# Performance work log

Hardware: AMD Instinct MI355X
Metric: run time of the kernel (lower is better)

Reference implementation:

```python
import jax, jax.numpy as jnp
import numpy as np

N_HEAD = 16

def setup_inputs() -> dict:
    key = jax.random.key(0)
    k1, k2, k3, k4, k5 = jax.random.split(key, 5)
    B, S, D = 2, 2048, 1024
    return {
        "hidden_states": jax.random.normal(k1, (B, S, D), jnp.float32),
        "w_attn": jax.random.normal(k2, (D, 3 * D), jnp.float32) * 0.02,
        "b_attn": jax.random.normal(k3, (3 * D,), jnp.float32) * 0.02,
        "w_proj": jax.random.normal(k4, (D, D), jnp.float32) * 0.02,
        "b_proj": jax.random.normal(k5, (D,), jnp.float32) * 0.02,
    }

def reference(hidden_states, w_attn, b_attn, w_proj, b_proj):
    B, S, D = hidden_states.shape
    H = N_HEAD
    Dh = D // H
    qkv = hidden_states @ w_attn + b_attn              # [B,S,3D]
    q, k, v = jnp.split(qkv, 3, axis=-1)
    def split_heads(x):
        return x.reshape(B, S, H, Dh).transpose(0, 2, 1, 3)  # [B,H,S,Dh]
    q, k, v = split_heads(q), split_heads(k), split_heads(v)
    # scale=True: divide by sqrt(head_dim) (v.size(-1))
    scores = jnp.einsum("bhqd,bhkd->bhqk", q, k) / jnp.sqrt(jnp.float32(Dh))
    attn = jax.nn.softmax(scores, axis=-1)             # [B,H,S,S]
    out = jnp.einsum("bhqk,bhkd->bhqd", attn, v)       # [B,H,S,Dh]
    out = out.transpose(0, 2, 1, 3).reshape(B, S, D)   # merge heads
    return out @ w_proj + b_proj
```

## Files before the change

### kernel.cpp

```cpp
#include <hip/hip_runtime.h>
#include <hip/hip_bf16.h>

typedef __attribute__((ext_vector_type(8))) short bf16x8;
typedef __attribute__((ext_vector_type(4))) float f32x4;
typedef __attribute__((ext_vector_type(16))) float f32x16;

#define LOG2E 1.4426950408889634f

__device__ inline unsigned short f2bf(float f) {
  union { float f; unsigned u; } x; x.f = f;
  unsigned u = x.u;
  unsigned r = u + 0x7FFFu + ((u >> 16) & 1u);
  return (unsigned short)(r >> 16);
}

__device__ inline unsigned cvtpk(float lo, float hi) {
  unsigned r;
  asm("v_cvt_pk_bf16_f32 %0, %1, %2" : "=v"(r) : "v"(lo), "v"(hi));
  return r;
}

__device__ inline void gload16(const unsigned short* g, unsigned short* l) {
  __builtin_amdgcn_global_load_lds(
      (const __attribute__((address_space(1))) unsigned int*)g,
      (__attribute__((address_space(3))) unsigned int*)l, 16, 0, 0);
}

template <int J>
__device__ inline bf16x8 pack_pfrag(f32x16 p) {
  int X, Y, Z, W;
  asm("v_cvt_pk_bf16_f32 %0, %1, %2" : "=v"(X) : "v"(p[J + 0]), "v"(p[J + 1]));
  asm("v_cvt_pk_bf16_f32 %0, %1, %2" : "=v"(Y) : "v"(p[J + 2]), "v"(p[J + 3]));
  asm("v_cvt_pk_bf16_f32 %0, %1, %2" : "=v"(Z) : "v"(p[J + 4]), "v"(p[J + 5]));
  asm("v_cvt_pk_bf16_f32 %0, %1, %2" : "=v"(W) : "v"(p[J + 6]), "v"(p[J + 7]));
  asm("v_permlane32_swap_b32 %0, %1" : "+v"(X), "+v"(Z));
  asm("v_permlane32_swap_b32 %0, %1" : "+v"(Y), "+v"(W));
  union { int w[4]; bf16x8 v; } u;
  u.w[0] = X; u.w[1] = Y; u.w[2] = Z; u.w[3] = W;
  return u.v;
}

__global__ __launch_bounds__(256) void cvt_bf16(const float* __restrict__ X,
                                                unsigned short* __restrict__ Y, int n4) {
  int i = blockIdx.x * blockDim.x + threadIdx.x;
  int stride = gridDim.x * blockDim.x;
  for (; i < n4; i += stride) {
    float4 v = reinterpret_cast<const float4*>(X)[i];
    ushort4 o;
    o.x = f2bf(v.x); o.y = f2bf(v.y); o.z = f2bf(v.z); o.w = f2bf(v.w);
    reinterpret_cast<ushort4*>(Y)[i] = o;
  }
}

__global__ __launch_bounds__(256) void transpose_cvt(const float* __restrict__ W,
                                                     unsigned short* __restrict__ WT,
                                                     int K, int N) {
  __shared__ unsigned short Tl[64][72];
  const int t = threadIdx.x;
  const int n0 = blockIdx.x * 64, k0 = blockIdx.y * 64;
#pragma unroll
  for (int i = 0; i < 4; ++i) {
    int idx = t + i * 256;
    int r = idx >> 4, c4 = (idx & 15) << 2;
    float4 v = *reinterpret_cast<const float4*>(&W[(size_t)(k0 + r) * N + n0 + c4]);
    Tl[c4 + 0][r] = f2bf(v.x);
    Tl[c4 + 1][r] = f2bf(v.y);
    Tl[c4 + 2][r] = f2bf(v.z);
    Tl[c4 + 3][r] = f2bf(v.w);
  }
  __syncthreads();
#pragma unroll
  for (int i = 0; i < 2; ++i) {
    int idx = t + i * 256;
    int rr = idx >> 3, cc = (idx & 7) << 3;
    *reinterpret_cast<int4*>(&WT[(size_t)(n0 + rr) * K + k0 + cc]) =
        *reinterpret_cast<const int4*>(&Tl[rr][cc]);
  }
}

#define GST(bs, kt)                                                             \
  {                                                                             \
    const unsigned short* Ap = Ab + (kt) * 32;                                  \
    const unsigned short* Bp = Bb + (kt) * 32;                                  \
    _Pragma("unroll") for (int i = 0; i < 2; ++i) {                             \
      int row = i * 64 + wid * 16 + s_r;                                        \
      gload16(&Ap[(size_t)row * 1024 + s_c], &Al[bs][i * 2048 + wid * 512]);    \
      gload16(&Bp[(size_t)row * 1024 + s_c], &Bl[bs][i * 2048 + wid * 512]);    \
    }                                                                           \
  }

#define GBODY(br)                                                               \
  {                                                                             \
    bf16x8 af[4], bfv[4];                                                       \
    _Pragma("unroll") for (int mm = 0; mm < 4; ++mm) {                          \
      int row = wr + mm * 16 + lr;                                              \
      af[mm] = *reinterpret_cast<const bf16x8*>(                                \
          &Al[br][row * 32 + ((kq ^ (lr & 3)) << 3)]);                          \
    }                                                                           \
    _Pragma("unroll") for (int nn = 0; nn < 4; ++nn) {                          \
      int row = wc + nn * 16 + lr;                                              \
      bfv[nn] = *reinterpret_cast<const bf16x8*>(                               \
          &Bl[br][row * 32 + ((kq ^ (lr & 3)) << 3)]);                          \
    }                                                                           \
    _Pragma("unroll") for (int mm = 0; mm < 4; ++mm)                            \
      _Pragma("unroll") for (int nn = 0; nn < 4; ++nn)                          \
        acc[mm][nn] =                                                           \
            __builtin_amdgcn_mfma_f32_16x16x32_bf16(af[mm], bfv[nn],            \
                                                    acc[mm][nn], 0, 0, 0);      \
  }

#define VMC4 asm volatile("s_waitcnt vmcnt(4)" ::: "memory");
#define VMC0 asm volatile("s_waitcnt vmcnt(0)" ::: "memory");
#define BAR __builtin_amdgcn_s_barrier();

__global__ __launch_bounds__(256) void gemm_qkv_b(
    const unsigned short* __restrict__ A, const unsigned short* __restrict__ Bt,
    const float* __restrict__ bias,
    unsigned short* __restrict__ qw, unsigned short* __restrict__ kw,
    unsigned short* __restrict__ vtg) {
  __shared__ unsigned short Al[3][4096];
  __shared__ unsigned short Bl[3][4096];
  const int t = threadIdx.x, lane = t & 63, wid = t >> 6;
  const int wr = (wid >> 1) * 64, wc = (wid & 1) * 64;
  const int row0 = blockIdx.y * 128, col0 = blockIdx.x * 128;
  const int lr = lane & 15, kq = lane >> 4;
  const int s_r = lane >> 2;
  const int s_c = ((lane & 3) ^ (s_r & 3)) * 8;
  const unsigned short* Ab = A + (size_t)row0 * 1024;
  const unsigned short* Bb = Bt + (size_t)col0 * 1024;
  f32x4 acc[4][4] = {};

  GST(0, 0) GST(1, 1)
  VMC4 BAR
  for (int tt = 0; tt < 30; tt += 3) {
    GST(2, tt + 2) GBODY(0) VMC4 BAR
    GST(0, tt + 3) GBODY(1) VMC4 BAR
    GST(1, tt + 4) GBODY(2) VMC4 BAR
  }
  GBODY(0) VMC0 BAR
  GBODY(1)

  const int rbase = (lane >> 4) * 4;
#pragma unroll
  for (int mm = 0; mm < 4; ++mm) {
#pragma unroll
    for (int nn = 0; nn < 4; ++nn) {
      int c = col0 + wc + nn * 16 + lr;
      int which = c >> 10;
      int d = c & 1023;
      int h = d >> 6, dh = d & 63;
      float bv = bias[c];
      int m0 = row0 + wr + mm * 16 + rbase;
      int b = m0 >> 11, s0 = m0 & 2047;
      if (which == 2) {
        int kt = s0 >> 6, key0 = s0 & 63;
        ushort4 pv;
        pv.x = f2bf(acc[mm][nn][0] + bv);
        pv.y = f2bf(acc[mm][nn][1] + bv);
        pv.z = f2bf(acc[mm][nn][2] + bv);
        pv.w = f2bf(acc[mm][nn][3] + bv);
        *reinterpret_cast<ushort4*>(
            &vtg[(((size_t)(b * 16 + h) * 32 + kt) * 64 + dh) * 64 + key0]) = pv;
      } else {
        unsigned short* dst = (which == 0) ? qw : kw;
#pragma unroll
        for (int r = 0; r < 4; ++r)
          dst[(((size_t)b * 16 + h) * 2048 + (s0 + r)) * 64 + dh] = f2bf(acc[mm][nn][r] + bv);
      }
    }
  }
}

__global__ __launch_bounds__(256) void gemm_proj_b(
    const unsigned short* __restrict__ A, const unsigned short* __restrict__ Bt,
    const float* __restrict__ bias, float* __restrict__ out) {
  const int N = 1024;
  __shared__ unsigned short Al[3][4096];
  __shared__ unsigned short Bl[3][4096];
  const int t = threadIdx.x, lane = t & 63, wid = t >> 6;
  const int wr = (wid >> 1) * 64, wc = (wid & 1) * 64;
  const int row0 = blockIdx.y * 128, col0 = blockIdx.x * 128;
  const int lr = lane & 15, kq = lane >> 4;
  const int s_r = lane >> 2;
  const int s_c = ((lane & 3) ^ (s_r & 3)) * 8;
  const unsigned short* Ab = A + (size_t)row0 * 1024;
  const unsigned short* Bb = Bt + (size_t)col0 * 1024;
  f32x4 acc[4][4] = {};

  GST(0, 0) GST(1, 1)
  VMC4 BAR
  for (int tt = 0; tt < 30; tt += 3) {
    GST(2, tt + 2) GBODY(0) VMC4 BAR
    GST(0, tt + 3) GBODY(1) VMC4 BAR
    GST(1, tt + 4) GBODY(2) VMC4 BAR
  }
  GBODY(0) VMC0 BAR
  GBODY(1)

  const int rbase = (lane >> 4) * 4;
#pragma unroll
  for (int mm = 0; mm < 4; ++mm) {
#pragma unroll
    for (int nn = 0; nn < 4; ++nn) {
      int c = col0 + wc + nn * 16 + lr;
      float bv = bias[c];
#pragma unroll
      for (int r = 0; r < 4; ++r) {
        int m = row0 + wr + mm * 16 + rbase + r;
        out[(size_t)m * N + c] = acc[mm][nn][r] + bv;
      }
    }
  }
}

__global__ __launch_bounds__(512, 4) void attn_kernel(
    const unsigned short* __restrict__ qw, const unsigned short* __restrict__ kw,
    const unsigned short* __restrict__ vtg, unsigned short* __restrict__ ow) {
  __shared__ char smem[65536];
  unsigned short* KV = (unsigned short*)smem;
  unsigned short* Ol = (unsigned short*)smem;
  float* EX = (float*)(smem + 18432);
  const int t = threadIdx.x, lane = t & 63, wid = t >> 6;
  const int half = wid >> 2, wq = wid & 3;
  const int l31 = lane & 31, hi = lane >> 5;
  const int qt = blockIdx.x, bh = blockIdx.y;
  const int b = bh >> 4, h = bh & 15;
  const unsigned short* Qg = qw + (size_t)bh * 2048 * 64;
  const unsigned short* Kg = kw + (size_t)bh * 2048 * 64;
  const unsigned short* Vg = vtg + (size_t)bh * 32 * 4096;
  const int q0 = qt * 128 + wq * 32;
  const float F = 0.125f * LOG2E;
  const float mF = 16.0f * F;

  union { short s[8]; bf16x8 v; } one_u;
#pragma unroll
  for (int i = 0; i < 8; ++i) one_u.s[i] = (short)0x3F80;
  const bf16x8 ones = one_u.v;

  bf16x8 qf[4];
#pragma unroll
  for (int kc = 0; kc < 4; ++kc)
    qf[kc] = *reinterpret_cast<const bf16x8*>(&Qg[(q0 + l31) * 64 + kc * 16 + hi * 8]);

  f32x16 oA = {0,0,0,0,0,0,0,0,0,0,0,0,0,0,0,0};
  f32x16 oB = {0,0,0,0,0,0,0,0,0,0,0,0,0,0,0,0};
  f32x16 lC = {0,0,0,0,0,0,0,0,0,0,0,0,0,0,0,0};

  const int srow_lo = lane >> 3;
  const int scg = (lane & 7) ^ srow_lo;

#define STAGE(buf, kt)                                                              \
  {                                                                                 \
    const unsigned short* Kt = Kg + (size_t)(kt) * 4096;                            \
    const unsigned short* Vs = Vg + (size_t)(kt) * 4096;                            \
    unsigned short* Kl = KV + half * 16384 + (buf) * 8192;                          \
    unsigned short* Vl = Kl + 4096;                                                 \
    _Pragma("unroll") for (int i = 0; i < 2; ++i) {                                 \
      int chunk = wq * 2 + i;                                                       \
      int row = chunk * 8 + srow_lo;                                                \
      gload16(&Kt[row * 64 + scg * 8], &Kl[chunk * 512]);                           \
      gload16(&Vs[row * 64 + scg * 8], &Vl[chunk * 512]);                           \
    }                                                                               \
  }

  const int kt0 = half * 16;
  STAGE(0, kt0)

  for (int it = 0; it < 16; ++it) {
    const int cur = it & 1;
    if (it + 1 < 16) {
      STAGE(cur ^ 1, kt0 + it + 1)
      asm volatile("s_waitcnt vmcnt(4)" ::: "memory");
    } else {
      asm volatile("s_waitcnt vmcnt(0)" ::: "memory");
    }
    __builtin_amdgcn_s_barrier();
    const unsigned short* Kl = KV + half * 16384 + cur * 8192;
    const unsigned short* Vl = Kl + 4096;

    f32x16 sA = {0,0,0,0,0,0,0,0,0,0,0,0,0,0,0,0};
    f32x16 sB = {0,0,0,0,0,0,0,0,0,0,0,0,0,0,0,0};
    __builtin_amdgcn_s_setprio(1);
#pragma unroll
    for (int kc = 0; kc < 4; ++kc) {
      bf16x8 k0f = *reinterpret_cast<const bf16x8*>(
          &Kl[l31 * 64 + (((kc * 2 + hi) ^ (l31 & 7)) << 3)]);
      bf16x8 k1f = *reinterpret_cast<const bf16x8*>(
          &Kl[(32 + l31) * 64 + (((kc * 2 + hi) ^ (l31 & 7)) << 3)]);
      sA = __builtin_amdgcn_mfma_f32_32x32x16_bf16(k0f, qf[kc], sA, 0, 0, 0);
      sB = __builtin_amdgcn_mfma_f32_32x32x16_bf16(k1f, qf[kc], sB, 0, 0, 0);
    }
    __builtin_amdgcn_s_setprio(0);

#pragma unroll
    for (int j = 0; j < 16; ++j) {
      sA[j] = exp2f(sA[j] * F - mF);
      sB[j] = exp2f(sB[j] * F - mF);
    }

    bf16x8 pf0 = pack_pfrag<0>(sA);
    bf16x8 pf1 = pack_pfrag<8>(sA);
    bf16x8 pf2 = pack_pfrag<0>(sB);
    bf16x8 pf3 = pack_pfrag<8>(sB);

    __builtin_amdgcn_s_setprio(1);
#pragma unroll
    for (int c = 0; c < 4; ++c) {
      bf16x8 pf = (c == 0) ? pf0 : (c == 1) ? pf1 : (c == 2) ? pf2 : pf3;
      int g = c * 2 + hi;
      bf16x8 v0f = *reinterpret_cast<const bf16x8*>(
          &Vl[l31 * 64 + ((g ^ (l31 & 7)) << 3)]);
      bf16x8 v1f = *reinterpret_cast<const bf16x8*>(
          &Vl[(32 + l31) * 64 + ((g ^ (l31 & 7)) << 3)]);
      oA = __builtin_amdgcn_mfma_f32_32x32x16_bf16(v0f, pf, oA, 0, 0, 0);
      oB = __builtin_amdgcn_mfma_f32_32x32x16_bf16(v1f, pf, oB, 0, 0, 0);
      lC = __builtin_amdgcn_mfma_f32_32x32x16_bf16(ones, pf, lC, 0, 0, 0);
    }
    __builtin_amdgcn_s_setprio(0);
    __builtin_amdgcn_s_barrier();
  }
#undef STAGE

  __syncthreads();
  if (half == 1) {
    float* e = EX + ((size_t)(wq * 64 + lane)) * 34;
#pragma unroll
    for (int j = 0; j < 16; ++j) { e[j] = oA[j]; e[16 + j] = oB[j]; }
    e[32] = lC[0];
  }
  __syncthreads();
  if (half == 0) {
    const float* e = EX + ((size_t)(wq * 64 + lane)) * 34;
    float linv = 1.0f / (lC[0] + e[32]);
    unsigned short* orow_l = Ol + (wq * 32 + l31) * 72;
#pragma unroll
    for (int g = 0; g < 4; ++g) {
      float a0 = (oA[4 * g + 0] + e[4 * g + 0]) * linv;
      float a1v = (oA[4 * g + 1] + e[4 * g + 1]) * linv;
      float a2v = (oA[4 * g + 2] + e[4 * g + 2]) * linv;
      float a3v = (oA[4 * g + 3] + e[4 * g + 3]) * linv;
      uint2 w0; w0.x = cvtpk(a0, a1v); w0.y = cvtpk(a2v, a3v);
      *reinterpret_cast<uint2*>(&orow_l[8 * g + 4 * hi]) = w0;
      float b0 = (oB[4 * g + 0] + e[16 + 4 * g + 0]) * linv;
      float b1v = (oB[4 * g + 1] + e[16 + 4 * g + 1]) * linv;
      float b2v = (oB[4 * g + 2] + e[16 + 4 * g + 2]) * linv;
      float b3v = (oB[4 * g + 3] + e[16 + 4 * g + 3]) * linv;
      uint2 w1; w1.x = cvtpk(b0, b1v); w1.y = cvtpk(b2v, b3v);
      *reinterpret_cast<uint2*>(&orow_l[32 + 8 * g + 4 * hi]) = w1;
    }
  }
  __syncthreads();
#pragma unroll
  for (int i = 0; i < 2; ++i) {
    int idx = t + i * 512;
    int q = idx >> 3, ch = idx & 7;
    int4 v = *reinterpret_cast<const int4*>(&Ol[q * 72 + ch * 8]);
    *reinterpret_cast<int4*>(
        &ow[(((size_t)b * 2048 + qt * 128 + q) * 16 + h) * 64 + ch * 8]) = v;
  }
}

extern "C" void kernel_launch(void* const* d_in, const int* in_sizes, int n_in,
                              void* d_out, int out_size, void* d_ws, size_t ws_size,
                              hipStream_t stream) {
  const float* hs = (const float*)d_in[0];
  const float* w_attn = (const float*)d_in[1];
  const float* b_attn = (const float*)d_in[2];
  const float* w_proj = (const float*)d_in[3];
  const float* b_proj = (const float*)d_in[4];
  float* out = (float*)d_out;

  const size_t HEAD = (size_t)2 * 16 * 2048 * 64;
  unsigned short* qw = (unsigned short*)d_ws;
  unsigned short* kw = qw + HEAD;
  unsigned short* vtg = kw + HEAD;
  unsigned short* hs_b = vtg + HEAD;
  unsigned short* ow = hs_b;
  unsigned short* wT = hs_b + HEAD;
  unsigned short* pT = wT + (size_t)3072 * 1024;

  cvt_bf16<<<2048, 256, 0, stream>>>(hs, hs_b, 1048576);
  transpose_cvt<<<dim3(48, 16), 256, 0, stream>>>(w_attn, wT, 1024, 3072);
  transpose_cvt<<<dim3(16, 16), 256, 0, stream>>>(w_proj, pT, 1024, 1024);

  gemm_qkv_b<<<dim3(24, 32), 256, 0, stream>>>(hs_b, wT, b_attn, qw, kw, vtg);
  attn_kernel<<<dim3(16, 32), 512, 0, stream>>>(qw, kw, vtg, ow);
  gemm_proj_b<<<dim3(8, 32), 256, 0, stream>>>(ow, pT, b_proj, out);
}
```

Before: 141.1 us.

## Load V fragments directly from global, compute row sums in VALU, remap block order

```diff
diff --git a/kernel.cpp b/kernel.cpp
--- a/kernel.cpp
+++ b/kernel.cpp
@@ -122,7 +122,9 @@
   __shared__ unsigned short Bl[3][4096];
   const int t = threadIdx.x, lane = t & 63, wid = t >> 6;
   const int wr = (wid >> 1) * 64, wc = (wid & 1) * 64;
-  const int row0 = blockIdx.y * 128, col0 = blockIdx.x * 128;
+  const int orig = blockIdx.x + 24 * blockIdx.y;
+  const int nid = (orig & 7) * 96 + (orig >> 3);
+  const int row0 = (nid / 24) * 128, col0 = (nid % 24) * 128;
   const int lr = lane & 15, kq = lane >> 4;
   const int s_r = lane >> 2;
   const int s_c = ((lane & 3) ^ (s_r & 3)) * 8;
@@ -179,7 +181,9 @@
   __shared__ unsigned short Bl[3][4096];
   const int t = threadIdx.x, lane = t & 63, wid = t >> 6;
   const int wr = (wid >> 1) * 64, wc = (wid & 1) * 64;
-  const int row0 = blockIdx.y * 128, col0 = blockIdx.x * 128;
+  const int orig = blockIdx.x + 8 * blockIdx.y;
+  const int nid = (orig & 7) * 32 + (orig >> 3);
+  const int row0 = (nid >> 3) * 128, col0 = (nid & 7) * 128;
   const int lr = lane & 15, kq = lane >> 4;
   const int s_r = lane >> 2;
   const int s_c = ((lane & 3) ^ (s_r & 3)) * 8;
@@ -216,14 +220,16 @@
 __global__ __launch_bounds__(512, 4) void attn_kernel(
     const unsigned short* __restrict__ qw, const unsigned short* __restrict__ kw,
     const unsigned short* __restrict__ vtg, unsigned short* __restrict__ ow) {
-  __shared__ char smem[65536];
-  unsigned short* KV = (unsigned short*)smem;
+  __shared__ char smem[53248];
+  unsigned short* KB = (unsigned short*)smem;
   unsigned short* Ol = (unsigned short*)smem;
   float* EX = (float*)(smem + 18432);
   const int t = threadIdx.x, lane = t & 63, wid = t >> 6;
   const int half = wid >> 2, wq = wid & 3;
   const int l31 = lane & 31, hi = lane >> 5;
-  const int qt = blockIdx.x, bh = blockIdx.y;
+  const int orig = blockIdx.x + 16 * blockIdx.y;
+  const int nid = (orig & 7) * 64 + (orig >> 3);
+  const int qt = nid & 15, bh = nid >> 4;
   const int b = bh >> 4, h = bh & 15;
   const unsigned short* Qg = qw + (size_t)bh * 2048 * 64;
   const unsigned short* Kg = kw + (size_t)bh * 2048 * 64;
@@ -232,11 +238,6 @@
   const float F = 0.125f * LOG2E;
   const float mF = 16.0f * F;
 
-  union { short s[8]; bf16x8 v; } one_u;
-#pragma unroll
-  for (int i = 0; i < 8; ++i) one_u.s[i] = (short)0x3F80;
-  const bf16x8 ones = one_u.v;
-
   bf16x8 qf[4];
 #pragma unroll
   for (int kc = 0; kc < 4; ++kc)
@@ -244,39 +245,40 @@
 
   f32x16 oA = {0,0,0,0,0,0,0,0,0,0,0,0,0,0,0,0};
   f32x16 oB = {0,0,0,0,0,0,0,0,0,0,0,0,0,0,0,0};
-  f32x16 lC = {0,0,0,0,0,0,0,0,0,0,0,0,0,0,0,0};
+  float lrun = 0.f;
 
   const int srow_lo = lane >> 3;
   const int scg = (lane & 7) ^ srow_lo;
-
-#define STAGE(buf, kt)                                                              \
+  unsigned short* KBh = KB + half * 8192;
+
+#define KSTAGE(buf, kt)                                                             \
   {                                                                                 \
     const unsigned short* Kt = Kg + (size_t)(kt) * 4096;                            \
-    const unsigned short* Vs = Vg + (size_t)(kt) * 4096;                            \
-    unsigned short* Kl = KV + half * 16384 + (buf) * 8192;                          \
-    unsigned short* Vl = Kl + 4096;                                                 \
+    unsigned short* Kl = KBh + (buf) * 4096;                                        \
     _Pragma("unroll") for (int i = 0; i < 2; ++i) {                                 \
       int chunk = wq * 2 + i;                                                       \
       int row = chunk * 8 + srow_lo;                                                \
       gload16(&Kt[row * 64 + scg * 8], &Kl[chunk * 512]);                           \
-      gload16(&Vs[row * 64 + scg * 8], &Vl[chunk * 512]);                           \
     }                                                                               \
   }
 
   const int kt0 = half * 16;
-  STAGE(0, kt0)
+  KSTAGE(0, kt0)
 
   for (int it = 0; it < 16; ++it) {
     const int cur = it & 1;
-    if (it + 1 < 16) {
-      STAGE(cur ^ 1, kt0 + it + 1)
-      asm volatile("s_waitcnt vmcnt(4)" ::: "memory");
-    } else {
-      asm volatile("s_waitcnt vmcnt(0)" ::: "memory");
-    }
+    const unsigned short* Vt = Vg + (size_t)(kt0 + it) * 4096;
+    bf16x8 vf[8];
+#pragma unroll
+    for (int c = 0; c < 4; ++c) {
+      vf[2 * c] = *reinterpret_cast<const bf16x8*>(&Vt[l31 * 64 + (c * 2 + hi) * 8]);
+      vf[2 * c + 1] =
+          *reinterpret_cast<const bf16x8*>(&Vt[(32 + l31) * 64 + (c * 2 + hi) * 8]);
+    }
+    asm volatile("s_waitcnt vmcnt(8)" ::: "memory");
     __builtin_amdgcn_s_barrier();
-    const unsigned short* Kl = KV + half * 16384 + cur * 8192;
-    const unsigned short* Vl = Kl + 4096;
+    if (it + 1 < 16) KSTAGE(cur ^ 1, kt0 + it + 1)
+    const unsigned short* Kl = KBh + cur * 4096;
 
     f32x16 sA = {0,0,0,0,0,0,0,0,0,0,0,0,0,0,0,0};
     f32x16 sB = {0,0,0,0,0,0,0,0,0,0,0,0,0,0,0,0};
@@ -292,11 +294,19 @@
     }
     __builtin_amdgcn_s_setprio(0);
 
+    float rsv[16];
 #pragma unroll
     for (int j = 0; j < 16; ++j) {
-      sA[j] = exp2f(sA[j] * F - mF);
-      sB[j] = exp2f(sB[j] * F - mF);
-    }
+      float pa = exp2f(sA[j] * F - mF);
+      float pb = exp2f(sB[j] * F - mF);
+      sA[j] = pa; sB[j] = pb;
+      rsv[j] = pa + pb;
+    }
+#pragma unroll
+    for (int s = 8; s >= 1; s >>= 1)
+#pragma unroll
+      for (int j = 0; j < s; ++j) rsv[j] += rsv[j + s];
+    lrun += rsv[0] + __shfl_xor(rsv[0], 32);
 
     bf16x8 pf0 = pack_pfrag<0>(sA);
     bf16x8 pf1 = pack_pfrag<8>(sA);
@@ -304,34 +314,29 @@
     bf16x8 pf3 = pack_pfrag<8>(sB);
 
     __builtin_amdgcn_s_setprio(1);
-#pragma unroll
-    for (int c = 0; c < 4; ++c) {
-      bf16x8 pf = (c == 0) ? pf0 : (c == 1) ? pf1 : (c == 2) ? pf2 : pf3;
-      int g = c * 2 + hi;
-      bf16x8 v0f = *reinterpret_cast<const bf16x8*>(
-          &Vl[l31 * 64 + ((g ^ (l31 & 7)) << 3)]);
-      bf16x8 v1f = *reinterpret_cast<const bf16x8*>(
-          &Vl[(32 + l31) * 64 + ((g ^ (l31 & 7)) << 3)]);
-      oA = __builtin_amdgcn_mfma_f32_32x32x16_bf16(v0f, pf, oA, 0, 0, 0);
-      oB = __builtin_amdgcn_mfma_f32_32x32x16_bf16(v1f, pf, oB, 0, 0, 0);
-      lC = __builtin_amdgcn_mfma_f32_32x32x16_bf16(ones, pf, lC, 0, 0, 0);
-    }
+    oA = __builtin_amdgcn_mfma_f32_32x32x16_bf16(vf[0], pf0, oA, 0, 0, 0);
+    oB = __builtin_amdgcn_mfma_f32_32x32x16_bf16(vf[1], pf0, oB, 0, 0, 0);
+    oA = __builtin_amdgcn_mfma_f32_32x32x16_bf16(vf[2], pf1, oA, 0, 0, 0);
+    oB = __builtin_amdgcn_mfma_f32_32x32x16_bf16(vf[3], pf1, oB, 0, 0, 0);
+    oA = __builtin_amdgcn_mfma_f32_32x32x16_bf16(vf[4], pf2, oA, 0, 0, 0);
+    oB = __builtin_amdgcn_mfma_f32_32x32x16_bf16(vf[5], pf2, oB, 0, 0, 0);
+    oA = __builtin_amdgcn_mfma_f32_32x32x16_bf16(vf[6], pf3, oA, 0, 0, 0);
+    oB = __builtin_amdgcn_mfma_f32_32x32x16_bf16(vf[7], pf3, oB, 0, 0, 0);
     __builtin_amdgcn_s_setprio(0);
-    __builtin_amdgcn_s_barrier();
-  }
-#undef STAGE
+  }
+#undef KSTAGE
 
   __syncthreads();
   if (half == 1) {
     float* e = EX + ((size_t)(wq * 64 + lane)) * 34;
 #pragma unroll
     for (int j = 0; j < 16; ++j) { e[j] = oA[j]; e[16 + j] = oB[j]; }
-    e[32] = lC[0];
+    e[32] = lrun;
   }
   __syncthreads();
   if (half == 0) {
     const float* e = EX + ((size_t)(wq * 64 + lane)) * 34;
-    float linv = 1.0f / (lC[0] + e[32]);
+    float linv = 1.0f / (lrun + e[32]);
     unsigned short* orow_l = Ol + (wq * 32 + l31) * 72;
 #pragma unroll
     for (int g = 0; g < 4; ++g) {
```

Result: slower. 190.2 us (+34.7%).
